# Kernel tuning notes

Hardware: AMD Instinct MI355X
Metric: run time of the kernel (lower is better)

The kernel has to match this reference:

```python
import jax, jax.numpy as jnp
import numpy as np

WS = 14  # window size
NH = 12  # num heads
EPS = 1e-5  # torch LayerNorm eps


def _rel_idx(ws: int) -> np.ndarray:
    coords = np.stack(np.meshgrid(np.arange(ws), np.arange(ws), indexing='ij'))
    cf = coords.reshape(2, -1)                      # (2, N)
    rel = cf[:, :, None] - cf[:, None, :]           # (2, N, N)
    rel = rel.transpose(1, 2, 0).copy()
    rel[:, :, 0] += ws - 1
    rel[:, :, 1] += ws - 1
    rel[:, :, 0] *= 2 * ws - 1
    return rel.sum(-1)                              # (N, N) int


def _layernorm(x, w, b):
    mu = jnp.mean(x, axis=-1, keepdims=True)
    var = jnp.var(x, axis=-1, keepdims=True)
    return (x - mu) * jax.lax.rsqrt(var + EPS) * w + b


def setup_inputs() -> dict:
    key = jax.random.key(0)
    ks = jax.random.split(key, 8)
    d, dff = 768, 3072
    s = lambda k, shape, sc: jax.random.normal(k, shape, jnp.float32) * sc
    return {
        'x': jax.random.normal(ks[0], (8, d, 56, 56), jnp.float32),
        'norm1_w': jnp.ones((d,), jnp.float32),
        'norm1_b': jnp.zeros((d,), jnp.float32),
        'qkv_w': s(ks[1], (d, 3 * d), 0.02),
        'qkv_b': jnp.zeros((3 * d,), jnp.float32),
        'rel_bias_table': s(ks[2], ((2 * WS - 1) ** 2, NH), 0.02),
        'proj_w': s(ks[3], (d, d), 0.02),
        'proj_b': jnp.zeros((d,), jnp.float32),
        'norm2_w': jnp.ones((d,), jnp.float32),
        'norm2_b': jnp.zeros((d,), jnp.float32),
        'fc1_w': s(ks[4], (d, dff), 0.02),
        'fc1_b': jnp.zeros((dff,), jnp.float32),
        'fc2_w': s(ks[5], (dff, d), 0.02),
        'fc2_b': jnp.zeros((d,), jnp.float32),
        'gamma1': jnp.full((d,), 1e-5, jnp.float32),
        'gamma2': jnp.full((d,), 1e-5, jnp.float32),
    }


def reference(x, norm1_w, norm1_b, qkv_w, qkv_b, rel_bias_table, proj_w, proj_b,
              norm2_w, norm2_b, fc1_w, fc1_b, fc2_w, fc2_b, gamma1, gamma2):
    B, C, H, W = x.shape
    nh, hd = NH, C // NH
    N = WS * WS
    xs = jnp.transpose(x, (0, 2, 3, 1))             # B,H,W,C
    shortcut = xs
    h = _layernorm(xs, norm1_w, norm1_b)

    # window partition (H, W divisible by WS)
    hw = h.reshape(B, H // WS, WS, W // WS, WS, C)
    hw = jnp.transpose(hw, (0, 1, 3, 2, 4, 5)).reshape(-1, N, C)  # (Bw, N, C)

    qkv = hw @ qkv_w + qkv_b                        # (Bw, N, 3C)
    qkv = qkv.reshape(-1, N, 3, nh, hd)
    q, k, v = [jnp.transpose(qkv[:, :, i], (0, 2, 1, 3)) for i in range(3)]  # (Bw,nh,N,hd)

    attn = jnp.einsum('bhnd,bhmd->bhnm', q, k) * (hd ** -0.5)
    rel_idx = jnp.asarray(_rel_idx(WS))             # static (N,N)
    bias = rel_bias_table[rel_idx]                  # (N,N,nh)
    attn = attn + jnp.transpose(bias, (2, 0, 1))[None]
    attn = jax.nn.softmax(attn, axis=-1)

    out = jnp.einsum('bhnm,bhmd->bnhd', attn, v).reshape(-1, N, C)
    out = out @ proj_w + proj_b                     # (Bw, N, C)

    # window reverse
    out = out.reshape(B, H // WS, W // WS, WS, WS, C)
    out = jnp.transpose(out, (0, 1, 3, 2, 4, 5)).reshape(B, H, W, C)

    xs = shortcut + gamma1 * out
    h2 = _layernorm(xs, norm2_w, norm2_b)
    mlp = jax.nn.gelu(h2 @ fc1_w + fc1_b, approximate=False) @ fc2_w + fc2_b
    xs = xs + gamma2 * mlp
    return jnp.transpose(xs, (0, 3, 1, 2))          # B,C,H,W
```

## Files before the change

kernel.cpp:

```cpp
#include <hip/hip_runtime.h>
#include <cstdint>
#include <cstddef>


typedef unsigned short u16;
typedef short short8 __attribute__((ext_vector_type(8)));
typedef float floatx4 __attribute__((ext_vector_type(4)));

static __device__ __forceinline__ float bf2f(u16 u) {
  return __uint_as_float(((unsigned)u) << 16);
}
static __device__ __forceinline__ u16 f2bf(float f) {
  unsigned u = __float_as_uint(f);
  return (u16)((u + 0x7FFFu + ((u >> 16) & 1u)) >> 16);
}
static __device__ __forceinline__ float ldin(const void* p, size_t i, int isf) {
  return isf ? ((const float*)p)[i] : bf2f(((const u16*)p)[i]);
}
static __device__ __forceinline__ void gload_lds16(const void* g, void* l) {
  __builtin_amdgcn_global_load_lds(
      (const __attribute__((address_space(1))) void*)g,
      (__attribute__((address_space(3))) void*)l, 16, 0, 0);
}

__global__ __launch_bounds__(256) void detect_kernel(const u16* __restrict__ x,
                                                     int* __restrict__ flag) {
  __shared__ int tot;
  if (threadIdx.x == 0) tot = 0;
  __syncthreads();
  int cnt = 0;
  for (int i = threadIdx.x; i < 4096; i += 256) {
    int e = (x[i] >> 7) & 0xFF;
    if (e >= 0xC1) cnt++;
  }
  atomicAdd(&tot, cnt);
  __syncthreads();
  if (threadIdx.x == 0) flag[0] = (tot > 16) ? 1 : 0;
}

__global__ __launch_bounds__(256) void cvt_params_kernel(
    const void* n1w, const void* n1b, const void* qkvb, const void* projb,
    const void* n2w, const void* n2b, const void* fc1b, const void* fc2b,
    const void* g1, const void* g2, const void* bt, u16* __restrict__ P,
    const int* __restrict__ flag) {
  int isf = *flag;
  int i = blockIdx.x * 256 + threadIdx.x;
  const void* src; int off;
  if      (i < 768)   { src = n1w;   off = i; }
  else if (i < 1536)  { src = n1b;   off = i - 768; }
  else if (i < 3840)  { src = qkvb;  off = i - 1536; }
  else if (i < 4608)  { src = projb; off = i - 3840; }
  else if (i < 5376)  { src = n2w;   off = i - 4608; }
  else if (i < 6144)  { src = n2b;   off = i - 5376; }
  else if (i < 9216)  { src = fc1b;  off = i - 6144; }
  else if (i < 9984)  { src = fc2b;  off = i - 9216; }
  else if (i < 10752) { src = g1;    off = i - 9984; }
  else if (i < 11520) { src = g2;    off = i - 10752; }
  else if (i < 20268) { src = bt;    off = i - 11520; }
  else return;
  P[i] = f2bf(ldin(src, off, isf));
}

__global__ __launch_bounds__(256) void wtr_kernel(const void* __restrict__ W,
                                                  u16* __restrict__ WT,
                                                  int K, int N,
                                                  const int* __restrict__ flag) {
  int isf = *flag;
  __shared__ u16 tl[32][33];
  int tx = threadIdx.x, ty = threadIdx.y;
  int n0 = blockIdx.x * 32, k0 = blockIdx.y * 32;
#pragma unroll
  for (int j = 0; j < 32; j += 8)
    tl[ty + j][tx] = f2bf(ldin(W, (size_t)(k0 + ty + j) * N + n0 + tx, isf));
  __syncthreads();
#pragma unroll
  for (int j = 0; j < 32; j += 8)
    WT[(size_t)(n0 + ty + j) * K + k0 + tx] = tl[tx][ty + j];
}

__global__ __launch_bounds__(256) void tin_kernel(const void* __restrict__ x,
                                                  u16* __restrict__ sc,
                                                  const int* __restrict__ flag) {
  int isf = *flag;
  int cc = blockIdx.x, h = blockIdx.y, b = blockIdx.z;
  __shared__ u16 tile[64 * 57];
  int tid = threadIdx.x;
  for (int i = tid; i < 64 * 56; i += 256) {
    int ci = i / 56, w = i - ci * 56;
    tile[ci * 57 + w] =
        f2bf(ldin(x, (((size_t)b * 768 + cc * 64 + ci) * 56 + h) * 56 + w, isf));
  }
  __syncthreads();
  int hb = h / 14, hi = h - hb * 14;
  for (int i = tid; i < 56 * 64; i += 256) {
    int w = i >> 6, ci = i & 63;
    int wb = w / 14, wj = w - wb * 14;
    int r = (b * 16 + hb * 4 + wb) * 196 + hi * 14 + wj;
    sc[(size_t)r * 768 + cc * 64 + ci] = tile[ci * 57 + w];
  }
}

__global__ __launch_bounds__(256) void tout_kernel(const u16* __restrict__ src,
                                                   void* __restrict__ out,
                                                   const int* __restrict__ flag) {
  int isf = *flag;
  int cc = blockIdx.x, h = blockIdx.y, b = blockIdx.z;
  __shared__ u16 tile[64 * 57];
  int tid = threadIdx.x;
  int hb = h / 14, hi = h - hb * 14;
  for (int i = tid; i < 56 * 64; i += 256) {
    int w = i >> 6, ci = i & 63;
    int wb = w / 14, wj = w - wb * 14;
    int r = (b * 16 + hb * 4 + wb) * 196 + hi * 14 + wj;
    tile[ci * 57 + w] = src[(size_t)r * 768 + cc * 64 + ci];
  }
  __syncthreads();
  for (int i = tid; i < 64 * 56; i += 256) {
    int ci = i / 56, w = i - ci * 56;
    size_t o = (((size_t)b * 768 + cc * 64 + ci) * 56 + h) * 56 + w;
    if (isf) ((float*)out)[o] = bf2f(tile[ci * 57 + w]);
    else     ((u16*)out)[o]   = tile[ci * 57 + w];
  }
}

__global__ __launch_bounds__(256) void ln_kernel(const u16* __restrict__ xin,
                                                 const u16* __restrict__ wt,
                                                 const u16* __restrict__ bs,
                                                 u16* __restrict__ out) {
  int row = blockIdx.x, t = threadIdx.x;
  const u16* xr = xin + (size_t)row * 768;
  float v0 = bf2f(xr[t]), v1 = bf2f(xr[t + 256]), v2 = bf2f(xr[t + 512]);
  float s1 = v0 + v1 + v2;
  float s2 = v0 * v0 + v1 * v1 + v2 * v2;
#pragma unroll
  for (int off = 32; off > 0; off >>= 1) {
    s1 += __shfl_xor(s1, off);
    s2 += __shfl_xor(s2, off);
  }
  __shared__ float p1[4], p2[4];
  if ((t & 63) == 0) { p1[t >> 6] = s1; p2[t >> 6] = s2; }
  __syncthreads();
  float S1 = p1[0] + p1[1] + p1[2] + p1[3];
  float S2 = p2[0] + p2[1] + p2[2] + p2[3];
  float mu = S1 * (1.f / 768.f);
  float var = S2 * (1.f / 768.f) - mu * mu;
  float rs = rsqrtf(var + 1e-5f);
  u16* orow = out + (size_t)row * 768;
  orow[t]       = f2bf((v0 - mu) * rs * bf2f(wt[t])       + bf2f(bs[t]));
  orow[t + 256] = f2bf((v1 - mu) * rs * bf2f(wt[t + 256]) + bf2f(bs[t + 256]));
  orow[t + 512] = f2bf((v2 - mu) * rs * bf2f(wt[t + 512]) + bf2f(bs[t + 512]));
}

template <int EPI>
__global__ __launch_bounds__(256) void gemm_kernel(
    const u16* __restrict__ A, const u16* __restrict__ BT,
    const u16* __restrict__ bias, const u16* __restrict__ gamma,
    u16* out, int N, int K) {
  __shared__ u16 As[128 * 32];
  __shared__ u16 Bs[128 * 32];
  int tid = threadIdx.x;
  int w = tid >> 6, l = tid & 63;
  int lane15 = l & 15, quad = l >> 4;
  int m0 = blockIdx.y * 128, n0 = blockIdx.x * 128;
  int wm = w & 1, wn = w >> 1;
  floatx4 acc[4][4];
#pragma unroll
  for (int i = 0; i < 4; i++)
#pragma unroll
    for (int j = 0; j < 4; j++)
#pragma unroll
      for (int e = 0; e < 4; e++) acc[i][j][e] = 0.f;

  const u16* Abase = A + (size_t)m0 * K;
  const u16* Bbase = BT + (size_t)n0 * K;
  int rseg = l >> 2, ch = l & 3;

  for (int kt = 0; kt < K; kt += 32) {
    __syncthreads();
#pragma unroll
    for (int sI = 0; sI < 2; ++sI) {
      int s = w * 2 + sI;
      gload_lds16(Abase + (size_t)(s * 16 + rseg) * K + kt + ch * 8, &As[s * 512]);
      gload_lds16(Bbase + (size_t)(s * 16 + rseg) * K + kt + ch * 8, &Bs[s * 512]);
    }
    __syncthreads();
    short8 af[4], bf[4];
#pragma unroll
    for (int mi = 0; mi < 4; ++mi)
      af[mi] = *(const short8*)&As[(wm * 64 + mi * 16 + lane15) * 32 + quad * 8];
#pragma unroll
    for (int ni = 0; ni < 4; ++ni)
      bf[ni] = *(const short8*)&Bs[(wn * 64 + ni * 16 + lane15) * 32 + quad * 8];
#pragma unroll
    for (int mi = 0; mi < 4; ++mi)
#pragma unroll
      for (int ni = 0; ni < 4; ++ni)
        acc[mi][ni] = __builtin_amdgcn_mfma_f32_16x16x32_bf16(
            af[mi], bf[ni], acc[mi][ni], 0, 0, 0);
  }

#pragma unroll
  for (int mi = 0; mi < 4; ++mi) {
    int row0 = m0 + wm * 64 + mi * 16 + quad * 4;
#pragma unroll
    for (int ni = 0; ni < 4; ++ni) {
      int col = n0 + wn * 64 + ni * 16 + lane15;
      float bv = bf2f(bias[col]);
#pragma unroll
      for (int reg = 0; reg < 4; ++reg) {
        int row = row0 + reg;
        float v = acc[mi][ni][reg] + bv;
        size_t idx = (size_t)row * N + col;
        if (EPI == 0) {
          out[idx] = f2bf(v);
        } else if (EPI == 1) {
          out[idx] = f2bf(bf2f(out[idx]) + bf2f(gamma[col]) * v);
        } else {
          out[idx] = f2bf(0.5f * v * (1.f + erff(v * 0.70710678118f)));
        }
      }
    }
  }
}

__global__ __launch_bounds__(256) void attn_kernel(const u16* __restrict__ qkv,
                                                   const u16* __restrict__ btab,
                                                   u16* __restrict__ out) {
  __shared__ __align__(16) u16 VT[64 * 232];
  __shared__ __align__(16) u16 Pa[4 * 16 * 32];
  __shared__ float bS[729];
  int bid = blockIdx.x;
  int win = bid / 12, h = bid - win * 12;
  int tid = threadIdx.x, w = tid >> 6, l = tid & 63;
  int lane15 = l & 15, quad = l >> 4;
  const u16* qbase = qkv + (size_t)win * 196 * 2304;

  for (int i = tid; i < 64 * 28; i += 256) {
    int d = i / 28, m = i - d * 28;
    VT[d * 232 + 196 + m] = 0;
  }
  for (int i = tid; i < 196 * 64; i += 256) {
    int m = i >> 6, d = i & 63;
    VT[d * 232 + m] = qbase[(size_t)m * 2304 + 1536 + h * 64 + d];
  }
  for (int i = tid; i < 729; i += 256) bS[i] = bf2f(btab[i * 12 + h]);
  __syncthreads();

  u16* Pw = Pa + w * 512;
  for (int rt = w; rt < 13; rt += 4) {
    floatx4 acc[13];
#pragma unroll
    for (int nt = 0; nt < 13; ++nt)
#pragma unroll
      for (int e = 0; e < 4; ++e) acc[nt][e] = 0.f;

    int rq = rt * 16 + lane15;
    bool qok = rq < 196;
#pragma unroll
    for (int kk = 0; kk < 2; ++kk) {
      short8 qf;
      if (qok)
        qf = *(const short8*)&qbase[(size_t)rq * 2304 + h * 64 + kk * 32 + quad * 8];
      else
#pragma unroll
        for (int e = 0; e < 8; ++e) qf[e] = 0;
#pragma unroll
      for (int nt = 0; nt < 13; ++nt) {
        int n = nt * 16 + lane15;
        short8 kf = *(const short8*)&qbase[(size_t)n * 2304 + 768 + h * 64 + kk * 32 + quad * 8];
        acc[nt] = __builtin_amdgcn_mfma_f32_16x16x32_bf16(qf, kf, acc[nt], 0, 0, 0);
      }
    }

    int i1[4], j1[4]; bool rv[4]; float mx[4], sm[4];
#pragma unroll
    for (int reg = 0; reg < 4; ++reg) {
      int r = rt * 16 + quad * 4 + reg;
      i1[reg] = r / 14; j1[reg] = r - i1[reg] * 14;
      rv[reg] = r < 196; mx[reg] = -1e30f; sm[reg] = 0.f;
    }
#pragma unroll
    for (int nt = 0; nt < 13; ++nt) {
      int cc = nt * 16 + lane15;
      bool cv = cc < 196;
      int i2 = cc / 14, j2 = cc - i2 * 14;
#pragma unroll
      for (int reg = 0; reg < 4; ++reg) {
        float v;
        if (cv) {
          v = acc[nt][reg] * 0.125f;
          if (rv[reg]) v += bS[(i1[reg] - i2 + 13) * 27 + (j1[reg] - j2 + 13)];
        } else v = -1e30f;
        acc[nt][reg] = v;
        mx[reg] = fmaxf(mx[reg], v);
      }
    }
#pragma unroll
    for (int reg = 0; reg < 4; ++reg)
#pragma unroll
      for (int off = 1; off < 16; off <<= 1)
        mx[reg] = fmaxf(mx[reg], __shfl_xor(mx[reg], off));
#pragma unroll
    for (int nt = 0; nt < 13; ++nt)
#pragma unroll
      for (int reg = 0; reg < 4; ++reg) {
        float p = __expf(acc[nt][reg] - mx[reg]);
        acc[nt][reg] = p; sm[reg] += p;
      }
#pragma unroll
    for (int reg = 0; reg < 4; ++reg) {
#pragma unroll
      for (int off = 1; off < 16; off <<= 1) sm[reg] += __shfl_xor(sm[reg], off);
      sm[reg] = 1.f / sm[reg];
    }

    floatx4 oa[4];
#pragma unroll
    for (int dt = 0; dt < 4; ++dt)
#pragma unroll
      for (int e = 0; e < 4; ++e) oa[dt][e] = 0.f;
#pragma unroll
    for (int kk = 0; kk < 7; ++kk) {
#pragma unroll
      for (int p = 0; p < 2; ++p) {
        int nt = kk * 2 + p;
#pragma unroll
        for (int reg = 0; reg < 4; ++reg) {
          float v = (nt < 13) ? acc[nt][reg] * sm[reg] : 0.f;
          Pw[(quad * 4 + reg) * 32 + p * 16 + lane15] = f2bf(v);
        }
      }
      asm volatile("s_waitcnt lgkmcnt(0)" ::: "memory");
      short8 pf = *(const short8*)&Pw[lane15 * 32 + quad * 8];
#pragma unroll
      for (int dt = 0; dt < 4; ++dt) {
        short8 vf = *(const short8*)&VT[(dt * 16 + lane15) * 232 + kk * 32 + quad * 8];
        oa[dt] = __builtin_amdgcn_mfma_f32_16x16x32_bf16(pf, vf, oa[dt], 0, 0, 0);
      }
      asm volatile("s_waitcnt lgkmcnt(0)" ::: "memory");
    }
#pragma unroll
    for (int dt = 0; dt < 4; ++dt)
#pragma unroll
      for (int reg = 0; reg < 4; ++reg) {
        int r = rt * 16 + quad * 4 + reg;
        if (r < 196)
          out[((size_t)win * 196 + r) * 768 + h * 64 + dt * 16 + lane15] =
              f2bf(oa[dt][reg]);
      }
  }
}

extern "C" void kernel_launch(void* const* d_in, const int* in_sizes, int n_in,
                              void* d_out, int out_size, void* d_ws, size_t ws_size,
                              hipStream_t stream) {
  const void* x      = d_in[0];
  const void* n1w    = d_in[1];
  const void* n1b    = d_in[2];
  const void* qkv_w  = d_in[3];
  const void* qkv_b  = d_in[4];
  const void* btab   = d_in[5];
  const void* proj_w = d_in[6];
  const void* proj_b = d_in[7];
  const void* n2w    = d_in[8];
  const void* n2b    = d_in[9];
  const void* fc1_w  = d_in[10];
  const void* fc1_b  = d_in[11];
  const void* fc2_w  = d_in[12];
  const void* fc2_b  = d_in[13];
  const void* gamma1 = d_in[14];
  const void* gamma2 = d_in[15];
  (void)in_sizes; (void)n_in; (void)out_size;

  int c;
  if      (ws_size >= 245432576ull) c = 1;
  else if (ws_size >= 168362240ull) c = 2;
  else                              c = 4;
  const int R = 25088 / c;
  const int WN = 128 / c;

  char* ws = (char*)d_ws;
  int*  flag  = (int*)ws;
  u16*  P     = (u16*)(ws + 256);
  u16*  qkvT  = (u16*)(ws + 65792);
  u16*  projT = (u16*)(ws + 65792 + 3538944);
  u16*  fc1T  = (u16*)(ws + 65792 + 4718592);
  u16*  fc2T  = (u16*)(ws + 65792 + 9437184);
  const size_t B0 = 38535168;
  u16*  buf0  = (u16*)(ws + 14221568);
  u16*  buf1  = (u16*)(ws + 14221568 + B0);
  char* scr   = ws + 14221568 + 2 * B0;

  u16 *p_n1w = P, *p_n1b = P + 768, *p_qkvb = P + 1536, *p_projb = P + 3840;
  u16 *p_n2w = P + 4608, *p_n2b = P + 5376, *p_fc1b = P + 6144;
  u16 *p_fc2b = P + 9216, *p_g1 = P + 9984, *p_g2 = P + 10752, *p_bt = P + 11520;

  dim3 b256(256), bw(32, 8);
  detect_kernel<<<dim3(1), b256, 0, stream>>>((const u16*)x, flag);
  cvt_params_kernel<<<dim3(80), b256, 0, stream>>>(
      n1w, n1b, qkv_b, proj_b, n2w, n2b, fc1_b, fc2_b, gamma1, gamma2, btab,
      P, flag);
  wtr_kernel<<<dim3(72, 24), bw, 0, stream>>>(qkv_w, qkvT, 768, 2304, flag);
  wtr_kernel<<<dim3(24, 24), bw, 0, stream>>>(proj_w, projT, 768, 768, flag);
  wtr_kernel<<<dim3(96, 24), bw, 0, stream>>>(fc1_w, fc1T, 768, 3072, flag);
  wtr_kernel<<<dim3(24, 96), bw, 0, stream>>>(fc2_w, fc2T, 3072, 768, flag);

  tin_kernel<<<dim3(12, 56, 8), b256, 0, stream>>>(x, buf0, flag);
  ln_kernel<<<dim3(25088), b256, 0, stream>>>(buf0, p_n1w, p_n1b, buf1);

  for (int hc = 0; hc < c; ++hc) {
    size_t ro = (size_t)hc * R * 768;
    u16* qC = (u16*)scr;
    u16* aC = (u16*)(scr + (size_t)R * 4608);
    gemm_kernel<0><<<dim3(18, R / 128), b256, 0, stream>>>(
        buf1 + ro, qkvT, p_qkvb, nullptr, qC, 2304, 768);
    attn_kernel<<<dim3(WN * 12), b256, 0, stream>>>(qC, p_bt, aC);
    gemm_kernel<1><<<dim3(6, R / 128), b256, 0, stream>>>(
        aC, projT, p_projb, p_g1, buf0 + ro, 768, 768);
  }

  ln_kernel<<<dim3(25088), b256, 0, stream>>>(buf0, p_n2w, p_n2b, buf1);

  for (int hc = 0; hc < c; ++hc) {
    size_t ro = (size_t)hc * R * 768;
    u16* gC = (u16*)scr;
    gemm_kernel<2><<<dim3(24, R / 128), b256, 0, stream>>>(
        buf1 + ro, fc1T, p_fc1b, nullptr, gC, 3072, 768);
    gemm_kernel<1><<<dim3(6, R / 128), b256, 0, stream>>>(
        gC, fc2T, p_fc2b, p_g2, buf0 + ro, 768, 3072);
  }

  tout_kernel<<<dim3(12, 56, 8), b256, 0, stream>>>(buf0, d_out, flag);
}
```

Baseline: 1.094 ms.

## Swizzle GEMM block order for L2 reuse and double-buffer attention P tile

```diff
diff --git a/kernel.cpp b/kernel.cpp
--- a/kernel.cpp
+++ b/kernel.cpp
@@ -155,13 +155,18 @@
 __global__ __launch_bounds__(256) void gemm_kernel(
     const u16* __restrict__ A, const u16* __restrict__ BT,
     const u16* __restrict__ bias, const u16* __restrict__ gamma,
-    u16* out, int N, int K) {
+    u16* out, int N, int K, int NX, int NY) {
+  int bid = blockIdx.x;
+  int r8 = bid & 7, q = bid >> 3;
+  int xb = q % NX, yb = (q / NX) * 8 + r8;
+  if (yb >= NY) return;
+
   __shared__ u16 As[128 * 32];
   __shared__ u16 Bs[128 * 32];
   int tid = threadIdx.x;
   int w = tid >> 6, l = tid & 63;
   int lane15 = l & 15, quad = l >> 4;
-  int m0 = blockIdx.y * 128, n0 = blockIdx.x * 128;
+  int m0 = yb * 128, n0 = xb * 128;
   int wm = w & 1, wn = w >> 1;
   floatx4 acc[4][4];
 #pragma unroll
@@ -227,7 +232,7 @@
                                                    const u16* __restrict__ btab,
                                                    u16* __restrict__ out) {
   __shared__ __align__(16) u16 VT[64 * 232];
-  __shared__ __align__(16) u16 Pa[4 * 16 * 32];
+  __shared__ __align__(16) u16 Pa[4 * 2 * 512];
   __shared__ float bS[729];
   int bid = blockIdx.x;
   int win = bid / 12, h = bid - win * 12;
@@ -246,7 +251,7 @@
   for (int i = tid; i < 729; i += 256) bS[i] = bf2f(btab[i * 12 + h]);
   __syncthreads();
 
-  u16* Pw = Pa + w * 512;
+  u16* Pw = Pa + w * 1024;
   for (int rt = w; rt < 13; rt += 4) {
     floatx4 acc[13];
 #pragma unroll
@@ -321,23 +326,23 @@
       for (int e = 0; e < 4; ++e) oa[dt][e] = 0.f;
 #pragma unroll
     for (int kk = 0; kk < 7; ++kk) {
+      u16* Pb = Pw + (kk & 1) * 512;
 #pragma unroll
       for (int p = 0; p < 2; ++p) {
         int nt = kk * 2 + p;
 #pragma unroll
         for (int reg = 0; reg < 4; ++reg) {
           float v = (nt < 13) ? acc[nt][reg] * sm[reg] : 0.f;
-          Pw[(quad * 4 + reg) * 32 + p * 16 + lane15] = f2bf(v);
+          Pb[(quad * 4 + reg) * 32 + p * 16 + lane15] = f2bf(v);
         }
       }
       asm volatile("s_waitcnt lgkmcnt(0)" ::: "memory");
-      short8 pf = *(const short8*)&Pw[lane15 * 32 + quad * 8];
+      short8 pf = *(const short8*)&Pb[lane15 * 32 + quad * 8];
 #pragma unroll
       for (int dt = 0; dt < 4; ++dt) {
         short8 vf = *(const short8*)&VT[(dt * 16 + lane15) * 232 + kk * 32 + quad * 8];
         oa[dt] = __builtin_amdgcn_mfma_f32_16x16x32_bf16(pf, vf, oa[dt], 0, 0, 0);
       }
-      asm volatile("s_waitcnt lgkmcnt(0)" ::: "memory");
     }
 #pragma unroll
     for (int dt = 0; dt < 4; ++dt)
@@ -350,6 +355,8 @@
       }
   }
 }
+
+static inline int gemm_grid(int NX, int NY) { return NX * ((NY + 7) / 8) * 8; }
 
 extern "C" void kernel_launch(void* const* d_in, const int* in_sizes, int n_in,
                               void* d_out, int out_size, void* d_ws, size_t ws_size,
@@ -378,6 +385,7 @@
   else                              c = 4;
   const int R = 25088 / c;
   const int WN = 128 / c;
+  const int NY = R / 128;
 
   char* ws = (char*)d_ws;
   int*  flag  = (int*)ws;
@@ -412,11 +420,11 @@
     size_t ro = (size_t)hc * R * 768;
     u16* qC = (u16*)scr;
     u16* aC = (u16*)(scr + (size_t)R * 4608);
-    gemm_kernel<0><<<dim3(18, R / 128), b256, 0, stream>>>(
-        buf1 + ro, qkvT, p_qkvb, nullptr, qC, 2304, 768);
+    gemm_kernel<0><<<dim3(gemm_grid(18, NY)), b256, 0, stream>>>(
+        buf1 + ro, qkvT, p_qkvb, nullptr, qC, 2304, 768, 18, NY);
     attn_kernel<<<dim3(WN * 12), b256, 0, stream>>>(qC, p_bt, aC);
-    gemm_kernel<1><<<dim3(6, R / 128), b256, 0, stream>>>(
-        aC, projT, p_projb, p_g1, buf0 + ro, 768, 768);
+    gemm_kernel<1><<<dim3(gemm_grid(6, NY)), b256, 0, stream>>>(
+        aC, projT, p_projb, p_g1, buf0 + ro, 768, 768, 6, NY);
   }
 
   ln_kernel<<<dim3(25088), b256, 0, stream>>>(buf0, p_n2w, p_n2b, buf1);
@@ -424,10 +432,10 @@
   for (int hc = 0; hc < c; ++hc) {
     size_t ro = (size_t)hc * R * 768;
     u16* gC = (u16*)scr;
-    gemm_kernel<2><<<dim3(24, R / 128), b256, 0, stream>>>(
-        buf1 + ro, fc1T, p_fc1b, nullptr, gC, 3072, 768);
-    gemm_kernel<1><<<dim3(6, R / 128), b256, 0, stream>>>(
-        gC, fc2T, p_fc2b, p_g2, buf0 + ro, 768, 3072);
+    gemm_kernel<2><<<dim3(gemm_grid(24, NY)), b256, 0, stream>>>(
+        buf1 + ro, fc1T, p_fc1b, nullptr, gC, 3072, 768, 24, NY);
+    gemm_kernel<1><<<dim3(gemm_grid(6, NY)), b256, 0, stream>>>(
+        gC, fc2T, p_fc2b, p_g2, buf0 + ro, 768, 3072, 6, NY);
   }
 
   tout_kernel<<<dim3(12, 56, 8), b256, 0, stream>>>(buf0, d_out, flag);
```

Result: faster. 1.051 ms (-4.0%).
